# Optimization experiments

Measured on AMD Instinct MI355X. Metric: run time of the kernel, lower is better.

The kernel has to match this reference:

```python
import jax, jax.numpy as jnp
import numpy as np

EPS = 1e-5
B, L, DM, DI, DR, DS, K = 1, 1024, 2048, 4096, 128, 16, 3
DT_MAX, DT_MIN, DT_FLOOR = 0.1, 0.001, 1e-4


def setup_inputs() -> dict:
    key = jax.random.key(0)
    ks = jax.random.split(key, 10)
    sc = lambda k, sh, s=0.02: (jax.random.normal(k, sh, jnp.float32) * s)
    # dt_proj bias init (softplus-inverse of dt sampled log-uniform in [dt_min, dt_max])
    dt = jnp.exp(jax.random.uniform(ks[7], (DI,), jnp.float32)
                 * (np.log(DT_MAX) - np.log(DT_MIN)) + np.log(DT_MIN))
    dt = jnp.clip(dt, DT_FLOOR, None)
    inv_dt = dt + jnp.log(-jnp.expm1(-dt))
    dt_std = DR ** (-0.5)  # dt_rank**-0.5 * dt_scale
    return {
        "x": jax.random.normal(ks[0], (B, L, DM), jnp.float32),
        "h": jnp.zeros((B, L, DI, DS), jnp.float32),
        "norm_w": jnp.ones((DM,), jnp.float32),
        "in_proj_w": sc(ks[1], (2 * DI, DM)),
        "conv_w": sc(ks[2], (DI, 1, K), 0.1),      # depthwise: (out=DI, in/groups=1, K)
        "conv_b": jnp.zeros((DI,), jnp.float32),
        "x_proj_w": sc(ks[3], (DR + 2 * DS, DI)),
        "dt_proj_w": jax.random.uniform(ks[4], (DI, DR), jnp.float32, -dt_std, dt_std),
        "dt_proj_b": inv_dt,
        "A_log": jnp.log(jnp.tile(jnp.arange(1, DS + 1, dtype=jnp.float32), (DI, 1))),
        "D": jnp.ones((DI,), jnp.float32),
        "out_proj_w": sc(ks[5], (DM, DI)),
    }


def reference(x, h, norm_w, in_proj_w, conv_w, conv_b, x_proj_w,
              dt_proj_w, dt_proj_b, A_log, D, out_proj_w):
    # RMSNorm
    xn = x * jax.lax.rsqrt(jnp.mean(x * x, axis=-1, keepdims=True) + EPS) * norm_w
    # in_proj -> split into x-branch and gate z
    xz = xn @ in_proj_w.T                      # (B,L,2*DI)
    xs, z = xz[..., :DI], xz[..., DI:]
    # depthwise conv over sequence (padding preserves L for odd K)
    xc = jax.lax.conv_general_dilated(
        jnp.transpose(xs, (0, 2, 1)), conv_w, (1,), [((K - 1) // 2, (K - 1) // 2)],
        dimension_numbers=("NCH", "OIH", "NCH"), feature_group_count=DI)
    xc = jnp.transpose(xc, (0, 2, 1)) + conv_b  # (B,L,DI)
    xc = jax.nn.silu(xc)
    # ssm_step (elementwise over L; h is per-position state)
    A = -jnp.exp(A_log)                        # (DI,DS)
    dBC = xc @ x_proj_w.T                      # (B,L,DR+2*DS)
    delta = jax.nn.softplus(dBC[..., :DR] @ dt_proj_w.T + dt_proj_b)  # (B,L,DI)
    Bm = dBC[..., DR:DR + DS]                  # (B,L,DS)
    Cm = dBC[..., DR + DS:]                    # (B,L,DS)
    deltaA = jnp.exp(delta[..., None] * A)     # (B,L,DI,DS)
    BX = delta[..., None] * Bm[:, :, None, :] * xc[..., None]  # (B,L,DI,DS)
    h_new = deltaA * h + BX                    # (B,L,DI,DS)
    y = jnp.einsum("blds,bls->bld", h_new, Cm) + D * xc
    out = (y * jax.nn.silu(z)) @ out_proj_w.T + xn  # residual adds normed x
    return out, h_new
```

## Files before the change

### kernel.cpp

```cpp
#include <hip/hip_runtime.h>
#include <hip/hip_bf16.h>
#include <math.h>

#define L_   1024
#define DM_  2048
#define DI_  4096
#define DR_  128
#define DS_  16
#define DBC_ 160

typedef __attribute__((ext_vector_type(4))) float f32x4;
typedef __attribute__((ext_vector_type(8))) short s16x8;

__device__ inline unsigned short f2b(float f) {
  unsigned int u = __float_as_uint(f);
  u += 0x7fffu + ((u >> 16) & 1u);
  return (unsigned short)(u >> 16);
}

__device__ inline void gload_lds16(const void* g, void* l) {
  __builtin_amdgcn_global_load_lds(
      (const __attribute__((address_space(1))) void*)g,
      (__attribute__((address_space(3))) void*)l, 16, 0, 0);
}

__launch_bounds__(256)
__global__ void rmsnorm_kernel(const float* __restrict__ x, const float* __restrict__ w,
                               float* __restrict__ xn, unsigned short* __restrict__ xnb) {
  int l = blockIdx.x;
  const float4* xr = (const float4*)(x + (size_t)l * DM_);
  const float4* wr = (const float4*)w;
  float4 v0 = xr[threadIdx.x];
  float4 v1 = xr[threadIdx.x + 256];
  float ss = v0.x*v0.x + v0.y*v0.y + v0.z*v0.z + v0.w*v0.w
           + v1.x*v1.x + v1.y*v1.y + v1.z*v1.z + v1.w*v1.w;
  for (int off = 32; off > 0; off >>= 1) ss += __shfl_down(ss, off, 64);
  __shared__ float sbuf[4];
  int lane = threadIdx.x & 63, wid = threadIdx.x >> 6;
  if (lane == 0) sbuf[wid] = ss;
  __syncthreads();
  float tot = sbuf[0] + sbuf[1] + sbuf[2] + sbuf[3];
  float scale = rsqrtf(tot / (float)DM_ + 1e-5f);
  float4 w0 = wr[threadIdx.x], w1 = wr[threadIdx.x + 256];
  float4 o0, o1;
  o0.x = v0.x * scale * w0.x; o0.y = v0.y * scale * w0.y;
  o0.z = v0.z * scale * w0.z; o0.w = v0.w * scale * w0.w;
  o1.x = v1.x * scale * w1.x; o1.y = v1.y * scale * w1.y;
  o1.z = v1.z * scale * w1.z; o1.w = v1.w * scale * w1.w;
  float4* outr = (float4*)(xn + (size_t)l * DM_);
  outr[threadIdx.x] = o0;
  outr[threadIdx.x + 256] = o1;
  uint2 p0, p1;
  p0.x = (unsigned)f2b(o0.x) | ((unsigned)f2b(o0.y) << 16);
  p0.y = (unsigned)f2b(o0.z) | ((unsigned)f2b(o0.w) << 16);
  p1.x = (unsigned)f2b(o1.x) | ((unsigned)f2b(o1.y) << 16);
  p1.y = (unsigned)f2b(o1.z) | ((unsigned)f2b(o1.w) << 16);
  uint2* ob = (uint2*)(xnb + (size_t)l * DM_);
  ob[threadIdx.x] = p0;
  ob[threadIdx.x + 256] = p1;
}

__launch_bounds__(256)
__global__ void f32_to_bf16_kernel(const float* __restrict__ in, unsigned short* __restrict__ out, int n4) {
  int i = blockIdx.x * 256 + threadIdx.x;
  if (i >= n4) return;
  float4 v = ((const float4*)in)[i];
  uint2 p;
  p.x = (unsigned)f2b(v.x) | ((unsigned)f2b(v.y) << 16);
  p.y = (unsigned)f2b(v.z) | ((unsigned)f2b(v.w) << 16);
  ((uint2*)out)[i] = p;
}

__launch_bounds__(256)
__global__ void dbc_to_bf16_kernel(const float* __restrict__ dBC, unsigned short* __restrict__ dtb) {
  int i = blockIdx.x * 256 + threadIdx.x;
  int l = i >> 7, j = i & 127;
  dtb[i] = f2b(dBC[(size_t)l * DBC_ + j]);
}

template<int EPI>
__launch_bounds__(256)
__global__ void gemm_bf16_mfma(const unsigned short* __restrict__ A,
                               const unsigned short* __restrict__ W,
                               float* __restrict__ C, int M, int N, int K,
                               const float* __restrict__ aux) {
  __shared__ unsigned short As[128 * 32];
  __shared__ unsigned short Ws[128 * 32];
  int bm = blockIdx.y * 128, bn = blockIdx.x * 128;
  int tid = threadIdx.x;
  int w = tid >> 6, lane = tid & 63;
  int wr = (w >> 1) * 64, wc = (w & 1) * 64;
  f32x4 acc[4][4];
#pragma unroll
  for (int m = 0; m < 4; m++)
#pragma unroll
    for (int n = 0; n < 4; n++) acc[m][n] = (f32x4){0.f, 0.f, 0.f, 0.f};

  int kb = lane >> 4, r = lane & 15;
  for (int k0 = 0; k0 < K; k0 += 32) {
#pragma unroll
    for (int i = 0; i < 2; i++) {
      int ch = (i * 4 + w) * 64 + lane;
      int row = ch >> 2, kc = ch & 3;
      gload_lds16(A + (size_t)(bm + row) * K + k0 + kc * 8, As + ch * 8);
      gload_lds16(W + (size_t)(bn + row) * K + k0 + kc * 8, Ws + ch * 8);
    }
    asm volatile("s_waitcnt vmcnt(0)" ::: "memory");
    __syncthreads();
    s16x8 a[4], b[4];
#pragma unroll
    for (int m = 0; m < 4; m++)
      a[m] = *(const s16x8*)(As + (wr + m * 16 + r) * 32 + kb * 8);
#pragma unroll
    for (int n = 0; n < 4; n++)
      b[n] = *(const s16x8*)(Ws + (wc + n * 16 + r) * 32 + kb * 8);
#pragma unroll
    for (int m = 0; m < 4; m++)
#pragma unroll
      for (int n = 0; n < 4; n++)
        acc[m][n] = __builtin_amdgcn_mfma_f32_16x16x32_bf16(a[m], b[n], acc[m][n], 0, 0, 0);
    __syncthreads();
  }
  int q = lane >> 4;
#pragma unroll
  for (int m = 0; m < 4; m++) {
#pragma unroll
    for (int n = 0; n < 4; n++) {
#pragma unroll
      for (int j = 0; j < 4; j++) {
        int row = bm + wr + m * 16 + q * 4 + j;
        int col = bn + wc + n * 16 + r;
        float v = acc[m][n][j];
        if (EPI == 1) {
          v += aux[col];
          v = fmaxf(v, 0.f) + log1pf(__expf(-fabsf(v)));
        }
        if (EPI == 2) v += aux[(size_t)row * N + col];
        C[(size_t)row * N + col] = v;
      }
    }
  }
}

template<int EPI>
__launch_bounds__(256)
__global__ void gemm_bf16_mfma_bm64(const unsigned short* __restrict__ A,
                                    const unsigned short* __restrict__ W,
                                    float* __restrict__ C, int M, int N, int K,
                                    const float* __restrict__ aux) {
  __shared__ unsigned short As[64 * 32];
  __shared__ unsigned short Ws[128 * 32];
  int bm = blockIdx.y * 64, bn = blockIdx.x * 128;
  int tid = threadIdx.x;
  int w = tid >> 6, lane = tid & 63;
  int wr = (w >> 1) * 32, wc = (w & 1) * 64;
  f32x4 acc[2][4];
#pragma unroll
  for (int m = 0; m < 2; m++)
#pragma unroll
    for (int n = 0; n < 4; n++) acc[m][n] = (f32x4){0.f, 0.f, 0.f, 0.f};

  int kb = lane >> 4, r = lane & 15;
  for (int k0 = 0; k0 < K; k0 += 32) {
    {
      int ch = w * 64 + lane;
      int row = ch >> 2, kc = ch & 3;
      gload_lds16(A + (size_t)(bm + row) * K + k0 + kc * 8, As + ch * 8);
    }
#pragma unroll
    for (int i = 0; i < 2; i++) {
      int ch = (i * 4 + w) * 64 + lane;
      int row = ch >> 2, kc = ch & 3;
      gload_lds16(W + (size_t)(bn + row) * K + k0 + kc * 8, Ws + ch * 8);
    }
    asm volatile("s_waitcnt vmcnt(0)" ::: "memory");
    __syncthreads();
    s16x8 a[2], b[4];
#pragma unroll
    for (int m = 0; m < 2; m++)
      a[m] = *(const s16x8*)(As + (wr + m * 16 + r) * 32 + kb * 8);
#pragma unroll
    for (int n = 0; n < 4; n++)
      b[n] = *(const s16x8*)(Ws + (wc + n * 16 + r) * 32 + kb * 8);
#pragma unroll
    for (int m = 0; m < 2; m++)
#pragma unroll
      for (int n = 0; n < 4; n++)
        acc[m][n] = __builtin_amdgcn_mfma_f32_16x16x32_bf16(a[m], b[n], acc[m][n], 0, 0, 0);
    __syncthreads();
  }
  int q = lane >> 4;
#pragma unroll
  for (int m = 0; m < 2; m++) {
#pragma unroll
    for (int n = 0; n < 4; n++) {
#pragma unroll
      for (int j = 0; j < 4; j++) {
        int row = bm + wr + m * 16 + q * 4 + j;
        int col = bn + wc + n * 16 + r;
        float v = acc[m][n][j];
        if (EPI == 2) v += aux[(size_t)row * N + col];
        C[(size_t)row * N + col] = v;
      }
    }
  }
}

__launch_bounds__(256)
__global__ void conv_silu_kernel(const float* __restrict__ xz, const float* __restrict__ cw,
                                 const float* __restrict__ cb, float* __restrict__ xc) {
  int idx = blockIdx.x * 256 + threadIdx.x;
  int l = idx >> 12, d = idx & (DI_ - 1);
  float w0 = cw[d * 3 + 0], w1 = cw[d * 3 + 1], w2 = cw[d * 3 + 2];
  float acc = cb[d];
  const float* base = xz + d;
  if (l > 0)      acc = fmaf(w0, base[(size_t)(l - 1) * (2 * DI_)], acc);
  acc = fmaf(w1, base[(size_t)l * (2 * DI_)], acc);
  if (l < L_ - 1) acc = fmaf(w2, base[(size_t)(l + 1) * (2 * DI_)], acc);
  float sig = 1.f / (1.f + __expf(-acc));
  xc[idx] = acc * sig;
}

__global__ void negexp_kernel(const float* __restrict__ a, float* __restrict__ o, int n) {
  int i = blockIdx.x * 256 + threadIdx.x;
  if (i < n) o[i] = -__expf(a[i]);
}

__launch_bounds__(256)
__global__ void xproj_stage1(const float* __restrict__ xc, const float* __restrict__ W,
                             float* __restrict__ part) {
  __shared__ float xcs[64][68];
  __shared__ float Ws[160][68];
  int k0 = blockIdx.x * 256;
  int l0 = blockIdx.y * 64;
  int tid = threadIdx.x;
  int rg = tid >> 4;
  int cg = tid & 15;
  float acc[4][10] = {};
  for (int kc = 0; kc < 256; kc += 64) {
    for (int i = tid; i < 64 * 16; i += 256) {
      int row = i >> 4, c4 = (i & 15) * 4;
      *(float4*)&xcs[row][c4] = *(const float4*)&xc[(size_t)(l0 + row) * DI_ + k0 + kc + c4];
    }
    for (int i = tid; i < 160 * 16; i += 256) {
      int row = i >> 4, c4 = (i & 15) * 4;
      *(float4*)&Ws[row][c4] = *(const float4*)&W[(size_t)row * DI_ + k0 + kc + c4];
    }
    __syncthreads();
#pragma unroll 4
    for (int k = 0; k < 64; k += 4) {
      float4 xa[4];
#pragma unroll
      for (int i = 0; i < 4; i++) xa[i] = *(const float4*)&xcs[rg * 4 + i][k];
#pragma unroll
      for (int j = 0; j < 10; j++) {
        float4 wv = *(const float4*)&Ws[cg * 10 + j][k];
#pragma unroll
        for (int i = 0; i < 4; i++) {
          float s = acc[i][j];
          s = fmaf(xa[i].x, wv.x, s);
          s = fmaf(xa[i].y, wv.y, s);
          s = fmaf(xa[i].z, wv.z, s);
          s = fmaf(xa[i].w, wv.w, s);
          acc[i][j] = s;
        }
      }
    }
    __syncthreads();
  }
  float* pb = part + ((size_t)blockIdx.x * L_ + l0) * DBC_;
#pragma unroll
  for (int i = 0; i < 4; i++)
#pragma unroll
    for (int j = 0; j < 10; j++)
      pb[(size_t)(rg * 4 + i) * DBC_ + cg * 10 + j] = acc[i][j];
}

__launch_bounds__(256)
__global__ void xproj_stage2(const float* __restrict__ part, float* __restrict__ dBC) {
  int i = blockIdx.x * 256 + threadIdx.x;
  float s = 0.f;
#pragma unroll
  for (int sp = 0; sp < 16; sp++) s += part[(size_t)sp * (L_ * DBC_) + i];
  dBC[i] = s;
}

__launch_bounds__(256)
__global__ void ssm_kernel2(const float* __restrict__ xz, const float* __restrict__ xc,
                            const float* __restrict__ dBC, const float* __restrict__ delta,
                            const float* __restrict__ h, const float* __restrict__ An,
                            const float* __restrict__ Dp, float* __restrict__ h_out,
                            unsigned short* __restrict__ yzb) {
  int pair = threadIdx.x >> 2;
  int q = threadIdx.x & 3;
  for (int base = blockIdx.x * 64; base < L_ * DI_; base += gridDim.x * 64) {
    int idx = base + pair;
    int l = idx >> 12, d = idx & (DI_ - 1);
    float dv = delta[idx];
    float xv = xc[idx];
    float4 hv = *(const float4*)(h + (size_t)idx * DS_ + q * 4);
    float4 Av = *(const float4*)(An + (size_t)d * DS_ + q * 4);
    float4 Bv = *(const float4*)(dBC + (size_t)l * DBC_ + DR_ + q * 4);
    float4 Cv = *(const float4*)(dBC + (size_t)l * DBC_ + DR_ + DS_ + q * 4);
    float4 hn;
    hn.x = __expf(dv * Av.x) * hv.x + dv * Bv.x * xv;
    hn.y = __expf(dv * Av.y) * hv.y + dv * Bv.y * xv;
    hn.z = __expf(dv * Av.z) * hv.z + dv * Bv.z * xv;
    hn.w = __expf(dv * Av.w) * hv.w + dv * Bv.w * xv;
    *(float4*)(h_out + (size_t)idx * DS_ + q * 4) = hn;
    float y = hn.x * Cv.x + hn.y * Cv.y + hn.z * Cv.z + hn.w * Cv.w;
    y += __shfl_xor(y, 1, 64);
    y += __shfl_xor(y, 2, 64);
    if (q == 0) {
      y = fmaf(Dp[d], xv, y);
      float zv = xz[(size_t)l * (2 * DI_) + DI_ + d];
      float sig = 1.f / (1.f + __expf(-zv));
      yzb[idx] = f2b(y * zv * sig);
    }
  }
}

extern "C" void kernel_launch(void* const* d_in, const int* in_sizes, int n_in,
                              void* d_out, int out_size, void* d_ws, size_t ws_size,
                              hipStream_t stream) {
  const float* x         = (const float*)d_in[0];
  const float* h         = (const float*)d_in[1];
  const float* norm_w    = (const float*)d_in[2];
  const float* in_proj_w = (const float*)d_in[3];
  const float* conv_w    = (const float*)d_in[4];
  const float* conv_b    = (const float*)d_in[5];
  const float* x_proj_w  = (const float*)d_in[6];
  const float* dt_proj_w = (const float*)d_in[7];
  const float* dt_proj_b = (const float*)d_in[8];
  const float* A_log     = (const float*)d_in[9];
  const float* Dvec      = (const float*)d_in[10];
  const float* out_projw = (const float*)d_in[11];

  float* out   = (float*)d_out;
  float* h_out = out + (size_t)L_ * DM_;

  float* ws    = (float*)d_ws;
  float* xn    = ws;
  float* xz    = xn    + (size_t)L_ * DM_;
  float* xc    = xz    + (size_t)L_ * 2 * DI_;
  float* dBC   = xc    + (size_t)L_ * DI_;
  float* delta = dBC   + (size_t)L_ * DBC_;
  float* An    = delta + (size_t)L_ * DI_;
  float* part  = An    + (size_t)DI_ * DS_;
  unsigned short* xnb  = (unsigned short*)(part + (size_t)16 * L_ * DBC_);
  unsigned short* wib  = xnb  + (size_t)L_ * DM_;
  unsigned short* wob  = wib  + (size_t)2 * DI_ * DM_;
  unsigned short* yzb  = wob  + (size_t)DM_ * DI_;
  unsigned short* dtb  = yzb  + (size_t)L_ * DI_;
  unsigned short* dtwb = dtb  + (size_t)L_ * DR_;

  rmsnorm_kernel<<<L_, 256, 0, stream>>>(x, norm_w, xn, xnb);
  f32_to_bf16_kernel<<<(2 * DI_ * DM_ / 4 + 255) / 256, 256, 0, stream>>>(in_proj_w, wib, 2 * DI_ * DM_ / 4);
  f32_to_bf16_kernel<<<(DM_ * DI_ / 4 + 255) / 256, 256, 0, stream>>>(out_projw, wob, DM_ * DI_ / 4);
  f32_to_bf16_kernel<<<(DI_ * DR_ / 4 + 255) / 256, 256, 0, stream>>>(dt_proj_w, dtwb, DI_ * DR_ / 4);
  gemm_bf16_mfma<0><<<dim3(2 * DI_ / 128, L_ / 128), 256, 0, stream>>>(
      xnb, wib, xz, L_, 2 * DI_, DM_, nullptr);
  conv_silu_kernel<<<L_ * DI_ / 256, 256, 0, stream>>>(xz, conv_w, conv_b, xc);
  negexp_kernel<<<(DI_ * DS_) / 256, 256, 0, stream>>>(A_log, An, DI_ * DS_);
  xproj_stage1<<<dim3(16, 16), 256, 0, stream>>>(xc, x_proj_w, part);
  xproj_stage2<<<L_ * DBC_ / 256, 256, 0, stream>>>(part, dBC);
  dbc_to_bf16_kernel<<<L_ * DR_ / 256, 256, 0, stream>>>(dBC, dtb);
  gemm_bf16_mfma<1><<<dim3(DI_ / 128, L_ / 128), 256, 0, stream>>>(
      dtb, dtwb, delta, L_, DI_, DR_, dt_proj_b);
  ssm_kernel2<<<4096, 256, 0, stream>>>(
      xz, xc, dBC, delta, h, An, Dvec, h_out, yzb);
  gemm_bf16_mfma_bm64<2><<<dim3(DM_ / 128, L_ / 64), 256, 0, stream>>>(
      yzb, wob, out, L_, DM_, DI_, xn);
}
```

Before: 393.0 us.

## Use bf16 MFMA for x_proj, store xc as bf16, and merge small kernels

```diff
diff --git a/kernel.cpp b/kernel.cpp
--- a/kernel.cpp
+++ b/kernel.cpp
@@ -16,6 +16,9 @@
   unsigned int u = __float_as_uint(f);
   u += 0x7fffu + ((u >> 16) & 1u);
   return (unsigned short)(u >> 16);
+}
+__device__ inline float b2f(unsigned short u) {
+  return __uint_as_float(((unsigned int)u) << 16);
 }
 
 __device__ inline void gload_lds16(const void* g, void* l) {
@@ -61,21 +64,26 @@
 }
 
 __launch_bounds__(256)
-__global__ void f32_to_bf16_kernel(const float* __restrict__ in, unsigned short* __restrict__ out, int n4) {
+__global__ void convert_weights_kernel(const float* __restrict__ w_in, const float* __restrict__ w_out,
+                                       const float* __restrict__ w_dt, const float* __restrict__ w_xp,
+                                       unsigned short* __restrict__ wib, unsigned short* __restrict__ wob,
+                                       unsigned short* __restrict__ dtwb, unsigned short* __restrict__ xpwb) {
+  const int N1 = 2 * DI_ * DM_ / 4;
+  const int N2 = DM_ * DI_ / 4;
+  const int N3 = DI_ * DR_ / 4;
+  const int N4 = DBC_ * DI_ / 4;
   int i = blockIdx.x * 256 + threadIdx.x;
-  if (i >= n4) return;
-  float4 v = ((const float4*)in)[i];
+  const float* src; unsigned short* dst; int off;
+  if (i < N1)                { src = w_in;  dst = wib;  off = i; }
+  else if (i < N1 + N2)      { src = w_out; dst = wob;  off = i - N1; }
+  else if (i < N1 + N2 + N3) { src = w_dt;  dst = dtwb; off = i - N1 - N2; }
+  else if (i < N1 + N2 + N3 + N4) { src = w_xp; dst = xpwb; off = i - N1 - N2 - N3; }
+  else return;
+  float4 v = ((const float4*)src)[off];
   uint2 p;
   p.x = (unsigned)f2b(v.x) | ((unsigned)f2b(v.y) << 16);
   p.y = (unsigned)f2b(v.z) | ((unsigned)f2b(v.w) << 16);
-  ((uint2*)out)[i] = p;
-}
-
-__launch_bounds__(256)
-__global__ void dbc_to_bf16_kernel(const float* __restrict__ dBC, unsigned short* __restrict__ dtb) {
-  int i = blockIdx.x * 256 + threadIdx.x;
-  int l = i >> 7, j = i & 127;
-  dtb[i] = f2b(dBC[(size_t)l * DBC_ + j]);
+  ((uint2*)dst)[off] = p;
 }
 
 template<int EPI>
@@ -208,7 +216,7 @@
 
 __launch_bounds__(256)
 __global__ void conv_silu_kernel(const float* __restrict__ xz, const float* __restrict__ cw,
-                                 const float* __restrict__ cb, float* __restrict__ xc) {
+                                 const float* __restrict__ cb, unsigned short* __restrict__ xcb) {
   int idx = blockIdx.x * 256 + threadIdx.x;
   int l = idx >> 12, d = idx & (DI_ - 1);
   float w0 = cw[d * 3 + 0], w1 = cw[d * 3 + 1], w2 = cw[d * 3 + 2];
@@ -218,77 +226,85 @@
   acc = fmaf(w1, base[(size_t)l * (2 * DI_)], acc);
   if (l < L_ - 1) acc = fmaf(w2, base[(size_t)(l + 1) * (2 * DI_)], acc);
   float sig = 1.f / (1.f + __expf(-acc));
-  xc[idx] = acc * sig;
-}
-
-__global__ void negexp_kernel(const float* __restrict__ a, float* __restrict__ o, int n) {
-  int i = blockIdx.x * 256 + threadIdx.x;
-  if (i < n) o[i] = -__expf(a[i]);
-}
-
-__launch_bounds__(256)
-__global__ void xproj_stage1(const float* __restrict__ xc, const float* __restrict__ W,
-                             float* __restrict__ part) {
-  __shared__ float xcs[64][68];
-  __shared__ float Ws[160][68];
-  int k0 = blockIdx.x * 256;
+  xcb[idx] = f2b(acc * sig);
+}
+
+__launch_bounds__(256)
+__global__ void xproj_stage1_mfma(const unsigned short* __restrict__ xcb,
+                                  const unsigned short* __restrict__ Wb,
+                                  float* __restrict__ part) {
+  __shared__ unsigned short As[64 * 32];
+  __shared__ unsigned short Bs[160 * 32];
+  int sp = blockIdx.x;
   int l0 = blockIdx.y * 64;
-  int tid = threadIdx.x;
-  int rg = tid >> 4;
-  int cg = tid & 15;
-  float acc[4][10] = {};
-  for (int kc = 0; kc < 256; kc += 64) {
-    for (int i = tid; i < 64 * 16; i += 256) {
-      int row = i >> 4, c4 = (i & 15) * 4;
-      *(float4*)&xcs[row][c4] = *(const float4*)&xc[(size_t)(l0 + row) * DI_ + k0 + kc + c4];
-    }
-    for (int i = tid; i < 160 * 16; i += 256) {
-      int row = i >> 4, c4 = (i & 15) * 4;
-      *(float4*)&Ws[row][c4] = *(const float4*)&W[(size_t)row * DI_ + k0 + kc + c4];
-    }
-    __syncthreads();
-#pragma unroll 4
-    for (int k = 0; k < 64; k += 4) {
-      float4 xa[4];
-#pragma unroll
-      for (int i = 0; i < 4; i++) xa[i] = *(const float4*)&xcs[rg * 4 + i][k];
-#pragma unroll
-      for (int j = 0; j < 10; j++) {
-        float4 wv = *(const float4*)&Ws[cg * 10 + j][k];
-#pragma unroll
-        for (int i = 0; i < 4; i++) {
-          float s = acc[i][j];
-          s = fmaf(xa[i].x, wv.x, s);
-          s = fmaf(xa[i].y, wv.y, s);
-          s = fmaf(xa[i].z, wv.z, s);
-          s = fmaf(xa[i].w, wv.w, s);
-          acc[i][j] = s;
-        }
+  int tid = threadIdx.x, w = tid >> 6, lane = tid & 63;
+  int wr = (w >> 1) * 32, wc = (w & 1) * 80;
+  int kb = lane >> 4, r = lane & 15;
+  f32x4 acc[2][5];
+#pragma unroll
+  for (int m = 0; m < 2; m++)
+#pragma unroll
+    for (int n = 0; n < 5; n++) acc[m][n] = (f32x4){0.f, 0.f, 0.f, 0.f};
+
+  for (int kt = 0; kt < 8; kt++) {
+    int k0 = sp * 256 + kt * 32;
+    {
+      int ch = w * 64 + lane;
+      int row = ch >> 2, kc = ch & 3;
+      gload_lds16(xcb + (size_t)(l0 + row) * DI_ + k0 + kc * 8, As + ch * 8);
+    }
+#pragma unroll
+    for (int i = 0; i < 3; i++) {
+      int g = i * 4 + w;
+      if (g < 10) {
+        int ch = g * 64 + lane;
+        int row = ch >> 2, kc = ch & 3;
+        gload_lds16(Wb + (size_t)row * DI_ + k0 + kc * 8, Bs + ch * 8);
       }
     }
-    __syncthreads();
-  }
-  float* pb = part + ((size_t)blockIdx.x * L_ + l0) * DBC_;
-#pragma unroll
-  for (int i = 0; i < 4; i++)
-#pragma unroll
-    for (int j = 0; j < 10; j++)
-      pb[(size_t)(rg * 4 + i) * DBC_ + cg * 10 + j] = acc[i][j];
-}
-
-__launch_bounds__(256)
-__global__ void xproj_stage2(const float* __restrict__ part, float* __restrict__ dBC) {
+    asm volatile("s_waitcnt vmcnt(0)" ::: "memory");
+    __syncthreads();
+    s16x8 a[2], b[5];
+#pragma unroll
+    for (int m = 0; m < 2; m++)
+      a[m] = *(const s16x8*)(As + (wr + m * 16 + r) * 32 + kb * 8);
+#pragma unroll
+    for (int n = 0; n < 5; n++)
+      b[n] = *(const s16x8*)(Bs + (wc + n * 16 + r) * 32 + kb * 8);
+#pragma unroll
+    for (int m = 0; m < 2; m++)
+#pragma unroll
+      for (int n = 0; n < 5; n++)
+        acc[m][n] = __builtin_amdgcn_mfma_f32_16x16x32_bf16(a[m], b[n], acc[m][n], 0, 0, 0);
+    __syncthreads();
+  }
+  int q = lane >> 4;
+  float* pb = part + (size_t)sp * (L_ * DBC_) + (size_t)l0 * DBC_;
+#pragma unroll
+  for (int m = 0; m < 2; m++)
+#pragma unroll
+    for (int n = 0; n < 5; n++)
+#pragma unroll
+      for (int j = 0; j < 4; j++)
+        pb[(size_t)(wr + m * 16 + q * 4 + j) * DBC_ + wc + n * 16 + r] = acc[m][n][j];
+}
+
+__launch_bounds__(256)
+__global__ void xproj_stage2(const float* __restrict__ part, float* __restrict__ dBC,
+                             unsigned short* __restrict__ dtb) {
   int i = blockIdx.x * 256 + threadIdx.x;
   float s = 0.f;
 #pragma unroll
   for (int sp = 0; sp < 16; sp++) s += part[(size_t)sp * (L_ * DBC_) + i];
   dBC[i] = s;
-}
-
-__launch_bounds__(256)
-__global__ void ssm_kernel2(const float* __restrict__ xz, const float* __restrict__ xc,
+  int l = i / DBC_, col = i - l * DBC_;
+  if (col < DR_) dtb[(size_t)l * DR_ + col] = f2b(s);
+}
+
+__launch_bounds__(256)
+__global__ void ssm_kernel2(const float* __restrict__ xz, const unsigned short* __restrict__ xcb,
                             const float* __restrict__ dBC, const float* __restrict__ delta,
-                            const float* __restrict__ h, const float* __restrict__ An,
+                            const float* __restrict__ h, const float* __restrict__ A_log,
                             const float* __restrict__ Dp, float* __restrict__ h_out,
                             unsigned short* __restrict__ yzb) {
   int pair = threadIdx.x >> 2;
@@ -297,16 +313,16 @@
     int idx = base + pair;
     int l = idx >> 12, d = idx & (DI_ - 1);
     float dv = delta[idx];
-    float xv = xc[idx];
+    float xv = b2f(xcb[idx]);
     float4 hv = *(const float4*)(h + (size_t)idx * DS_ + q * 4);
-    float4 Av = *(const float4*)(An + (size_t)d * DS_ + q * 4);
+    float4 Al = *(const float4*)(A_log + (size_t)d * DS_ + q * 4);
     float4 Bv = *(const float4*)(dBC + (size_t)l * DBC_ + DR_ + q * 4);
     float4 Cv = *(const float4*)(dBC + (size_t)l * DBC_ + DR_ + DS_ + q * 4);
     float4 hn;
-    hn.x = __expf(dv * Av.x) * hv.x + dv * Bv.x * xv;
-    hn.y = __expf(dv * Av.y) * hv.y + dv * Bv.y * xv;
-    hn.z = __expf(dv * Av.z) * hv.z + dv * Bv.z * xv;
-    hn.w = __expf(dv * Av.w) * hv.w + dv * Bv.w * xv;
+    hn.x = __expf(dv * -__expf(Al.x)) * hv.x + dv * Bv.x * xv;
+    hn.y = __expf(dv * -__expf(Al.y)) * hv.y + dv * Bv.y * xv;
+    hn.z = __expf(dv * -__expf(Al.z)) * hv.z + dv * Bv.z * xv;
+    hn.w = __expf(dv * -__expf(Al.w)) * hv.w + dv * Bv.w * xv;
     *(float4*)(h_out + (size_t)idx * DS_ + q * 4) = hn;
     float y = hn.x * Cv.x + hn.y * Cv.y + hn.z * Cv.z + hn.w * Cv.w;
     y += __shfl_xor(y, 1, 64);
@@ -342,33 +358,30 @@
   float* ws    = (float*)d_ws;
   float* xn    = ws;
   float* xz    = xn    + (size_t)L_ * DM_;
-  float* xc    = xz    + (size_t)L_ * 2 * DI_;
-  float* dBC   = xc    + (size_t)L_ * DI_;
+  float* dBC   = xz    + (size_t)L_ * 2 * DI_;
   float* delta = dBC   + (size_t)L_ * DBC_;
-  float* An    = delta + (size_t)L_ * DI_;
-  float* part  = An    + (size_t)DI_ * DS_;
+  float* part  = delta + (size_t)L_ * DI_;
   unsigned short* xnb  = (unsigned short*)(part + (size_t)16 * L_ * DBC_);
   unsigned short* wib  = xnb  + (size_t)L_ * DM_;
   unsigned short* wob  = wib  + (size_t)2 * DI_ * DM_;
   unsigned short* yzb  = wob  + (size_t)DM_ * DI_;
   unsigned short* dtb  = yzb  + (size_t)L_ * DI_;
   unsigned short* dtwb = dtb  + (size_t)L_ * DR_;
+  unsigned short* xpwb = dtwb + (size_t)DI_ * DR_;
+  unsigned short* xcb  = xpwb + (size_t)DBC_ * DI_;
 
   rmsnorm_kernel<<<L_, 256, 0, stream>>>(x, norm_w, xn, xnb);
-  f32_to_bf16_kernel<<<(2 * DI_ * DM_ / 4 + 255) / 256, 256, 0, stream>>>(in_proj_w, wib, 2 * DI_ * DM_ / 4);
-  f32_to_bf16_kernel<<<(DM_ * DI_ / 4 + 255) / 256, 256, 0, stream>>>(out_projw, wob, DM_ * DI_ / 4);
-  f32_to_bf16_kernel<<<(DI_ * DR_ / 4 + 255) / 256, 256, 0, stream>>>(dt_proj_w, dtwb, DI_ * DR_ / 4);
+  convert_weights_kernel<<<(2 * DI_ * DM_ + DM_ * DI_ + DI_ * DR_ + DBC_ * DI_) / 4 / 256, 256, 0, stream>>>(
+      in_proj_w, out_projw, dt_proj_w, x_proj_w, wib, wob, dtwb, xpwb);
   gemm_bf16_mfma<0><<<dim3(2 * DI_ / 128, L_ / 128), 256, 0, stream>>>(
       xnb, wib, xz, L_, 2 * DI_, DM_, nullptr);
-  conv_silu_kernel<<<L_ * DI_ / 256, 256, 0, stream>>>(xz, conv_w, conv_b, xc);
-  negexp_kernel<<<(DI_ * DS_) / 256, 256, 0, stream>>>(A_log, An, DI_ * DS_);
-  xproj_stage1<<<dim3(16, 16), 256, 0, stream>>>(xc, x_proj_w, part);
-  xproj_stage2<<<L_ * DBC_ / 256, 256, 0, stream>>>(part, dBC);
-  dbc_to_bf16_kernel<<<L_ * DR_ / 256, 256, 0, stream>>>(dBC, dtb);
+  conv_silu_kernel<<<L_ * DI_ / 256, 256, 0, stream>>>(xz, conv_w, conv_b, xcb);
+  xproj_stage1_mfma<<<dim3(16, 16), 256, 0, stream>>>(xcb, xpwb, part);
+  xproj_stage2<<<L_ * DBC_ / 256, 256, 0, stream>>>(part, dBC, dtb);
   gemm_bf16_mfma<1><<<dim3(DI_ / 128, L_ / 128), 256, 0, stream>>>(
       dtb, dtwb, delta, L_, DI_, DR_, dt_proj_b);
   ssm_kernel2<<<4096, 256, 0, stream>>>(
-      xz, xc, dBC, delta, h, An, Dvec, h_out, yzb);
+      xz, xcb, dBC, delta, h, A_log, Dvec, h_out, yzb);
   gemm_bf16_mfma_bm64<2><<<dim3(DM_ / 128, L_ / 64), 256, 0, stream>>>(
       yzb, wob, out, L_, DM_, DI_, xn);
 }
```

Measured after the change: 341.0 us. -13.2%, faster.
